# Performance work log

Hardware: AMD Instinct MI355X
Metric: run time of the kernel (lower is better)

Reference implementation:

```python
import jax, jax.numpy as jnp
import numpy as np

N_QUBITS = 10
Q_DEPTH = 6
MAX_LAYERS = 15
DIM = 2 ** N_QUBITS


def _apply_1q(s, U, w):
    # s: (B, 2^n) real statevector (circuit uses only H/RY/CNOT, all real).
    # Wire 0 is the most-significant bit (PennyLane convention).
    a, b = 2 ** w, 2 ** (N_QUBITS - 1 - w)
    s = s.reshape(-1, a, 2, b)
    if U.ndim == 2:  # gate shared across batch
        s = jnp.einsum('ij,Bajb->Baib', U, s)
    else:            # per-sample gate, U: (B,2,2)
        s = jnp.einsum('Bij,Bajb->Baib', U, s)
    return s.reshape(-1, DIM)


def _apply_cnot(s, c, t):
    # CNOT, control c < target t
    s = s.reshape(-1, 2 ** c, 2, 2 ** (t - c - 1), 2, 2 ** (N_QUBITS - 1 - t))
    s = jnp.stack([s[:, :, 0], jnp.flip(s[:, :, 1], axis=3)], axis=2)
    return s.reshape(-1, DIM)


def _ry(theta):
    # RY(theta) = [[cos t/2, -sin t/2], [sin t/2, cos t/2]]; theta scalar or (B,)
    c, si = jnp.cos(theta / 2.0), jnp.sin(theta / 2.0)
    return jnp.stack([jnp.stack([c, -si], -1), jnp.stack([si, c], -1)], -2)


def _quantum_net(q_in, q_params):
    # q_in: (B, n_qubits) rotation angles; q_params: (max_layers*n_qubits,)
    B = q_in.shape[0]
    qw = q_params.reshape(MAX_LAYERS, N_QUBITS)
    s = jnp.zeros((B, DIM), q_in.dtype).at[:, 0].set(1.0)  # |0...0>
    H = jnp.array([[1.0, 1.0], [1.0, -1.0]], q_in.dtype) / jnp.sqrt(jnp.asarray(2.0, q_in.dtype))
    for w in range(N_QUBITS):
        s = _apply_1q(s, H, w)
    for w in range(N_QUBITS):
        s = _apply_1q(s, _ry(q_in[:, w]), w)
    for k in range(Q_DEPTH):
        for i in range(0, N_QUBITS - 1, 2):
            s = _apply_cnot(s, i, i + 1)
        for i in range(1, N_QUBITS - 1, 2):
            s = _apply_cnot(s, i, i + 1)
        for w in range(N_QUBITS):
            s = _apply_1q(s, _ry(qw[k + 1, w]), w)
    probs = s * s
    # <Z_w> = P(bit_w = 0) - P(bit_w = 1)
    z = []
    for w in range(N_QUBITS):
        p = probs.reshape(-1, 2 ** w, 2, 2 ** (N_QUBITS - 1 - w)).sum(axis=(1, 3))
        z.append(p[:, 0] - p[:, 1])
    return jnp.stack(z, axis=1)  # (B, n_qubits)


def setup_inputs() -> dict:
    key = jax.random.key(0)
    ks = jax.random.split(key, 6)
    B, F, NQ, NC = 8192, 512, N_QUBITS, 2
    q_delta = 0.01
    return {
        'input_features': jax.random.normal(ks[0], (B, F), jnp.float32),
        'W_pre': jax.random.normal(ks[1], (NQ, F), jnp.float32) / np.sqrt(F),
        'b_pre': jnp.zeros((NQ,), jnp.float32),
        'q_params': q_delta * jax.random.normal(ks[2], (MAX_LAYERS * NQ,), jnp.float32),
        'W_post': jax.random.normal(ks[3], (NC, NQ), jnp.float32) / np.sqrt(NQ),
        'b_post': jnp.zeros((NC,), jnp.float32),
    }


def reference(input_features, W_pre, b_pre, q_params, W_post, b_post):
    pre_out = input_features @ W_pre.T + b_pre          # (B, n_qubits)
    q_in = jnp.tanh(pre_out) * (np.pi / 2.0)            # scale to [-pi/2, pi/2]
    q_out = _quantum_net(q_in, q_params)                # (B, n_qubits) PauliZ expvals
    return q_out @ W_post.T + b_post                    # (B, n_classes)
```

## Files before the change

kernel.cpp:

```cpp
#include <hip/hip_runtime.h>
#include <math.h>


#define NQ   10
#define NREG 16
#define DIM  1024

typedef _Float16 f16;
typedef _Float16 f16x8 __attribute__((ext_vector_type(8)));
typedef float    f32x4 __attribute__((ext_vector_type(4)));

template<int BB>
__device__ __forceinline__ void ry_lane(float (&s)[NREG], int lane, float c, float si) {
    float sgn = ((lane >> BB) & 1) ? si : -si;
    #pragma unroll
    for (int r = 0; r < NREG; ++r) {
        float o = __shfl_xor(s[r], 1 << BB);
        s[r] = fmaf(sgn, o, c * s[r]);
    }
}
template<int P>
__device__ __forceinline__ void ry_reg(float (&s)[NREG], float c, float si) {
    const int m = 1 << P;
    #pragma unroll
    for (int r = 0; r < NREG; ++r) {
        if ((r & m) == 0) {
            float a = s[r], b = s[r + m];
            s[r]     = fmaf(c, a, -si * b);
            s[r + m] = fmaf(si, a,  c * b);
        }
    }
}
__device__ __forceinline__ void cnot_5_6(float (&s)[NREG], int lane) {
    bool sel = (lane & 1) != 0;
    #pragma unroll
    for (int r = 0; r < 8; ++r) {
        float a = s[r], b = s[r + 8];
        s[r]     = sel ? b : a;
        s[r + 8] = sel ? a : b;
    }
}
template<int PC, int PT>
__device__ __forceinline__ void cnot_reg(float (&s)[NREG]) {
    #pragma unroll
    for (int r = 0; r < NREG; ++r) {
        if (((r >> PC) & 1) && !((r >> PT) & 1)) {
            float t = s[r];
            s[r] = s[r ^ (1 << PT)];
            s[r ^ (1 << PT)] = t;
        }
    }
}
__device__ __forceinline__ void perm_even(float (&s)[NREG], int lane) {
    int src = lane ^ (((((lane >> 5) & 1) << 4)) | ((((lane >> 3) & 1) << 2)) | (((lane >> 1) & 1)));
    #pragma unroll
    for (int r = 0; r < NREG; ++r) s[r] = __shfl(s[r], src);
}
__device__ __forceinline__ void perm_odd(float (&s)[NREG], int lane) {
    int src = lane ^ (((((lane >> 4) & 1) << 3)) | ((((lane >> 2) & 1) << 1)));
    #pragma unroll
    for (int r = 0; r < NREG; ++r) s[r] = __shfl(s[r], src);
}

#define APPLY_RY_ALL(CARR, SARR, BASE)                                        \
    { float c_, s_;                                                           \
      c_=__shfl(CARR,(BASE)+0); s_=__shfl(SARR,(BASE)+0); ry_lane<5>(s,lane,c_,s_); \
      c_=__shfl(CARR,(BASE)+1); s_=__shfl(SARR,(BASE)+1); ry_lane<4>(s,lane,c_,s_); \
      c_=__shfl(CARR,(BASE)+2); s_=__shfl(SARR,(BASE)+2); ry_lane<3>(s,lane,c_,s_); \
      c_=__shfl(CARR,(BASE)+3); s_=__shfl(SARR,(BASE)+3); ry_lane<2>(s,lane,c_,s_); \
      c_=__shfl(CARR,(BASE)+4); s_=__shfl(SARR,(BASE)+4); ry_lane<1>(s,lane,c_,s_); \
      c_=__shfl(CARR,(BASE)+5); s_=__shfl(SARR,(BASE)+5); ry_lane<0>(s,lane,c_,s_); \
      c_=__shfl(CARR,(BASE)+6); s_=__shfl(SARR,(BASE)+6); ry_reg<3>(s,c_,s_);       \
      c_=__shfl(CARR,(BASE)+7); s_=__shfl(SARR,(BASE)+7); ry_reg<2>(s,c_,s_);       \
      c_=__shfl(CARR,(BASE)+8); s_=__shfl(SARR,(BASE)+8); ry_reg<1>(s,c_,s_);       \
      c_=__shfl(CARR,(BASE)+9); s_=__shfl(SARR,(BASE)+9); ry_reg<0>(s,c_,s_); }

__device__ __forceinline__ void async16(const void* g, void* l) {
    __builtin_amdgcn_global_load_lds(
        (const __attribute__((address_space(1))) void*)g,
        (__attribute__((address_space(3))) void*)l, 16, 0, 0);
}

__global__ __launch_bounds__(256) void ka_prepare(
    const float* __restrict__ X, const float* __restrict__ Wpre,
    const float* __restrict__ bpre, const float* __restrict__ qp,
    f16* __restrict__ psi0, f16* __restrict__ Arm, float* __restrict__ z, int B)
{
    const int tid = threadIdx.x, lane = tid & 63, wv = tid >> 6;

    {
        int idx = blockIdx.x * 256 + tid;
        if (idx < 8192 * NQ) z[idx] = 0.0f;
    }

    {
        int sample = blockIdx.x * 4 + wv;
        if (sample < B) {
            const float* xrow = X + (size_t)sample * 512;
            float4 x0 = ((const float4*)xrow)[lane];
            float4 x1 = ((const float4*)xrow)[64 + lane];
            float acc[NQ];
            #pragma unroll
            for (int q = 0; q < NQ; ++q) {
                const float* wr = Wpre + q * 512;
                float4 w0 = ((const float4*)wr)[lane];
                float4 w1 = ((const float4*)wr)[64 + lane];
                float a = x0.x * w0.x;
                a = fmaf(x0.y, w0.y, a); a = fmaf(x0.z, w0.z, a); a = fmaf(x0.w, w0.w, a);
                a = fmaf(x1.x, w1.x, a); a = fmaf(x1.y, w1.y, a);
                a = fmaf(x1.z, w1.z, a); a = fmaf(x1.w, w1.w, a);
                acc[q] = a;
            }
            #pragma unroll
            for (int q = 0; q < NQ; ++q) {
                float v = acc[q];
                #pragma unroll
                for (int d = 32; d >= 1; d >>= 1) v += __shfl_xor(v, d);
                acc[q] = v;
            }
            float pre = acc[0];
            #pragma unroll
            for (int q = 1; q < NQ; ++q) pre = (lane == q) ? acc[q] : pre;
            float c45 = 0.0f, s45 = 0.0f;
            if (lane < NQ) {
                float th = tanhf(pre + bpre[lane]) * 1.5707963267948966f;
                sincosf(0.5f * th + 0.7853981633974483f, &s45, &c45);
            }
            float lv = 1.0f;
            #pragma unroll
            for (int w = 0; w < 6; ++w) {
                float f0 = __shfl(c45, w), f1 = __shfl(s45, w);
                lv *= ((lane >> (5 - w)) & 1) ? f1 : f0;
            }
            float c6 = __shfl(c45, 6), s6 = __shfl(s45, 6);
            float c7 = __shfl(c45, 7), s7 = __shfl(s45, 7);
            float c8 = __shfl(c45, 8), s8 = __shfl(s45, 8);
            float c9 = __shfl(c45, 9), s9 = __shfl(s45, 9);
            float g01[4] = {c6 * c7, c6 * s7, s6 * c7, s6 * s7};
            float g23[4] = {c8 * c9, c8 * s9, s8 * c9, s8 * s9};
            union { f16 h[16]; float4 v[2]; } u;
            #pragma unroll
            for (int r = 0; r < NREG; ++r)
                u.h[r] = (f16)(lv * g01[r >> 2] * g23[r & 3]);
            float4* dst = (float4*)((char*)psi0 + (size_t)sample * 2048 + lane * 32);
            dst[0] = u.v[0];
            dst[1] = u.v[1];
        }
    }

    if (wv < 2) {
        int row = blockIdx.x * 2 + wv;
        if (row < DIM) {
            float cw = 1.0f, swn = 0.0f;
            if (lane < 60) {
                float s_, c_;
                sincosf(0.5f * qp[10 + lane], &s_, &c_);
                cw = c_; swn = -s_;
            }
            float s[NREG];
            int srcLane = row >> 4, srcReg = row & 15;
            #pragma unroll
            for (int r = 0; r < NREG; ++r)
                s[r] = (lane == srcLane && r == srcReg) ? 1.0f : 0.0f;
            for (int kk = 6; kk >= 1; --kk) {
                APPLY_RY_ALL(cw, swn, (kk - 1) * 10);
                perm_odd(s, lane);
                cnot_5_6(s, lane);
                cnot_reg<2, 1>(s);
                perm_even(s, lane);
                cnot_reg<3, 2>(s);
                cnot_reg<1, 0>(s);
            }
            union { f16 h[16]; float4 v[2]; } u;
            #pragma unroll
            for (int r = 0; r < NREG; ++r) u.h[r] = (f16)s[r];
            float4* dst = (float4*)((char*)Arm + (size_t)row * 2048 + lane * 32);
            dst[0] = u.v[0];
            dst[1] = u.v[1];
        }
    }
}

__global__ __launch_bounds__(256) void kb_gemm_measure(
    const f16* __restrict__ psi0, const f16* __restrict__ Arm,
    float* __restrict__ z)
{
    __shared__ __align__(16) char smem[32768];
    const int tid = threadIdx.x, lane = tid & 63, wv = tid >> 6;
    const int mB = blockIdx.x & 63, nB = blockIdx.x >> 6;
    const size_t tM = (size_t)mB * 128, tN = (size_t)nB * 128;
    f16* As = (f16*)smem;
    f16* Bs = (f16*)(smem + 16384);
    const int wm = (wv >> 1) * 64, wn = (wv & 1) * 64;

    f32x4 acc[4][4] = {};

    const f16* ga[4]; const f16* gb[4]; int ldso[4];
    #pragma unroll
    for (int p = 0; p < 4; ++p) {
        int slot = p * 256 + tid;
        int row = slot >> 3, gp = slot & 7, g = gp ^ (row & 7);
        ga[p] = psi0 + (tM + row) * 1024 + g * 8;
        gb[p] = Arm  + (tN + row) * 1024 + g * 8;
        ldso[p] = slot * 16;
    }

    for (int kt = 0; kt < 1024; kt += 64) {
        __syncthreads();
        #pragma unroll
        for (int p = 0; p < 4; ++p) async16(ga[p] + kt, (char*)As + ldso[p]);
        #pragma unroll
        for (int p = 0; p < 4; ++p) async16(gb[p] + kt, (char*)Bs + ldso[p]);
        __syncthreads();
        #pragma unroll
        for (int ks = 0; ks < 2; ++ks) {
            f16x8 af[4], bf[4];
            const int gpb = ks * 4 + (lane >> 4);
            const int gpx = gpb ^ (lane & 7);
            #pragma unroll
            for (int i = 0; i < 4; ++i) {
                int rowA = wm + i * 16 + (lane & 15);
                af[i] = *(const f16x8*)(As + rowA * 64 + gpx * 8);
            }
            #pragma unroll
            for (int j = 0; j < 4; ++j) {
                int rowB = wn + j * 16 + (lane & 15);
                bf[j] = *(const f16x8*)(Bs + rowB * 64 + gpx * 8);
            }
            #pragma unroll
            for (int i = 0; i < 4; ++i)
                #pragma unroll
                for (int j = 0; j < 4; ++j)
                    acc[i][j] = __builtin_amdgcn_mfma_f32_16x16x32_f16(af[i], bf[j], acc[i][j], 0, 0, 0);
        }
    }

    __syncthreads();
    float* zbuf = (float*)smem;
    float* zb = zbuf + (wn ? 1280 : 0);
    const float sg0 = (nB & 4) ? -1.0f : 1.0f;
    const float sg1 = (nB & 2) ? -1.0f : 1.0f;
    const float sg2 = (nB & 1) ? -1.0f : 1.0f;
    const float sg3 = wn ? -1.0f : 1.0f;

    #pragma unroll
    for (int i = 0; i < 4; ++i) {
        #pragma unroll
        for (int t = 0; t < 4; ++t) {
            float p0 = acc[i][0][t] * acc[i][0][t];
            float p1 = acc[i][1][t] * acc[i][1][t];
            float p2 = acc[i][2][t] * acc[i][2][t];
            float p3 = acc[i][3][t] * acc[i][3][t];
            float t0  = (p0 + p1) + (p2 + p3);
            float tw5 = (p0 - p1) + (p2 - p3);
            float tw4 = (p0 + p1) - (p2 + p3);
            float s1 = __shfl_xor(t0, 1);
            float Av = t0 + s1;
            float Bv = (lane & 1) ? s1 - t0 : t0 - s1;
            float sA = __shfl_xor(Av, 2), sB = __shfl_xor(Bv, 2);
            float AP = Av + sA;
            float AM = (lane & 2) ? sA - Av : Av - sA;
            float BP = Bv + sB;
            float sAP = __shfl_xor(AP, 4), sAM = __shfl_xor(AM, 4), sBP = __shfl_xor(BP, 4);
            float APP = AP + sAP;
            float APM = (lane & 4) ? sAP - AP : AP - sAP;
            float AMP = AM + sAM;
            float BPP = BP + sBP;
            float a1 = __shfl_xor(APP, 8), a2 = __shfl_xor(APM, 8);
            float a3 = __shfl_xor(AMP, 8), a4 = __shfl_xor(BPP, 8);
            float T0 = APP + a1;
            float S6 = (lane & 8) ? a1 - APP : APP - a1;
            float S7 = APM + a2;
            float S8 = AMP + a3;
            float S9 = BPP + a4;
            float T5 = tw5, T4 = tw4;
            T5 += __shfl_xor(T5, 1); T5 += __shfl_xor(T5, 2);
            T5 += __shfl_xor(T5, 4); T5 += __shfl_xor(T5, 8);
            T4 += __shfl_xor(T4, 1); T4 += __shfl_xor(T4, 2);
            T4 += __shfl_xor(T4, 4); T4 += __shfl_xor(T4, 8);
            if ((lane & 15) == 0) {
                int row = wm + i * 16 + (lane >> 4) * 4 + t;
                float* d = zb + row * 10;
                d[0] = sg0 * T0; d[1] = sg1 * T0; d[2] = sg2 * T0; d[3] = sg3 * T0;
                d[4] = T4; d[5] = T5;
                d[6] = S6; d[7] = S7; d[8] = S8; d[9] = S9;
            }
        }
    }
    __syncthreads();
    for (int idx = tid; idx < 1280; idx += 256) {
        float v = zbuf[idx] + zbuf[1280 + idx];
        int row = idx / 10, w = idx - row * 10;
        atomicAdd(&z[((size_t)tM + row) * 10 + w], v);
    }
}

__global__ __launch_bounds__(256) void kc_post(
    const float* __restrict__ z, const float* __restrict__ Wpost,
    const float* __restrict__ bpost, float* __restrict__ out, int B)
{
    int gid = blockIdx.x * 256 + threadIdx.x;
    if (gid >= B) return;
    const float* zp = z + (size_t)gid * NQ;
    float o0 = bpost[0], o1 = bpost[1];
    #pragma unroll
    for (int w = 0; w < NQ; ++w) {
        float zw = zp[w];
        o0 = fmaf(zw, Wpost[w], o0);
        o1 = fmaf(zw, Wpost[NQ + w], o1);
    }
    out[(size_t)gid * 2 + 0] = o0;
    out[(size_t)gid * 2 + 1] = o1;
}

template<int BC, int BT>
__device__ __forceinline__ void cnot_lane(float (&s)[NREG], int lane) {
    int src = ((lane >> BC) & 1) ? (lane ^ (1 << BT)) : lane;
    #pragma unroll
    for (int r = 0; r < NREG; ++r) s[r] = __shfl(s[r], src);
}

__global__ __launch_bounds__(256) void hybrid_head_fallback(
    const float* __restrict__ X, const float* __restrict__ Wpre,
    const float* __restrict__ bpre, const float* __restrict__ qp,
    const float* __restrict__ Wpost, const float* __restrict__ bpost,
    float* __restrict__ out, int B)
{
    const int lane = threadIdx.x & 63;
    const int wave = threadIdx.x >> 6;
    const int sample = blockIdx.x * 4 + wave;
    if (sample >= B) return;

    const float* xrow = X + (size_t)sample * 512;
    float4 x0 = ((const float4*)xrow)[lane];
    float4 x1 = ((const float4*)xrow)[64 + lane];
    float acc[NQ];
    #pragma unroll
    for (int q = 0; q < NQ; ++q) {
        const float* wr = Wpre + q * 512;
        float4 w0 = ((const float4*)wr)[lane];
        float4 w1 = ((const float4*)wr)[64 + lane];
        float a = x0.x * w0.x;
        a = fmaf(x0.y, w0.y, a); a = fmaf(x0.z, w0.z, a); a = fmaf(x0.w, w0.w, a);
        a = fmaf(x1.x, w1.x, a); a = fmaf(x1.y, w1.y, a);
        a = fmaf(x1.z, w1.z, a); a = fmaf(x1.w, w1.w, a);
        acc[q] = a;
    }
    #pragma unroll
    for (int q = 0; q < NQ; ++q) {
        float v = acc[q];
        #pragma unroll
        for (int d = 32; d >= 1; d >>= 1) v += __shfl_xor(v, d);
        acc[q] = v;
    }
    float pre = acc[0];
    #pragma unroll
    for (int q = 1; q < NQ; ++q) pre = (lane == q) ? acc[q] : pre;
    float cth = 1.0f, sth = 0.0f;
    if (lane < NQ) {
        float th = tanhf(pre + bpre[lane]) * 1.5707963267948966f;
        sincosf(0.5f * th, &sth, &cth);
    }
    float cw = 1.0f, sw = 0.0f;
    if (lane < 60) sincosf(0.5f * qp[10 + lane], &sw, &cw);

    float s[NREG];
    #pragma unroll
    for (int r = 0; r < NREG; ++r) s[r] = 0.03125f;
    APPLY_RY_ALL(cth, sth, 0);
    for (int k = 0; k < 6; ++k) {
        perm_even(s, lane);
        cnot_reg<3, 2>(s);
        cnot_reg<1, 0>(s);
        perm_odd(s, lane);
        cnot_5_6(s, lane);
        cnot_reg<2, 1>(s);
        APPLY_RY_ALL(cw, sw, k * 10);
    }
    float p[NREG], tot = 0.0f;
    #pragma unroll
    for (int r = 0; r < NREG; ++r) { p[r] = s[r] * s[r]; tot += p[r]; }
    float z[NQ];
    #pragma unroll
    for (int w = 0; w < 6; ++w) z[w] = ((lane >> (5 - w)) & 1) ? -tot : tot;
    z[6] = z[7] = z[8] = z[9] = 0.0f;
    #pragma unroll
    for (int r = 0; r < NREG; ++r) {
        z[6] += ((r >> 3) & 1) ? -p[r] : p[r];
        z[7] += ((r >> 2) & 1) ? -p[r] : p[r];
        z[8] += ((r >> 1) & 1) ? -p[r] : p[r];
        z[9] += ((r >> 0) & 1) ? -p[r] : p[r];
    }
    #pragma unroll
    for (int w = 0; w < NQ; ++w) {
        float v = z[w];
        #pragma unroll
        for (int d = 32; d >= 1; d >>= 1) v += __shfl_xor(v, d);
        z[w] = v;
    }
    if (lane < 2) {
        const float* wp = Wpost + lane * NQ;
        float o = bpost[lane];
        #pragma unroll
        for (int w = 0; w < NQ; ++w) o = fmaf(z[w], wp[w], o);
        out[(size_t)sample * 2 + lane] = o;
    }
}

extern "C" void kernel_launch(void* const* d_in, const int* in_sizes, int n_in,
                              void* d_out, int out_size, void* d_ws, size_t ws_size,
                              hipStream_t stream) {
    const float* X     = (const float*)d_in[0];
    const float* Wpre  = (const float*)d_in[1];
    const float* bpre  = (const float*)d_in[2];
    const float* qp    = (const float*)d_in[3];
    const float* Wpost = (const float*)d_in[4];
    const float* bpost = (const float*)d_in[5];
    float* out = (float*)d_out;
    int B = in_sizes[0] / 512;

    size_t psi0_b = (size_t)B * DIM * sizeof(f16);
    size_t arm_b  = (size_t)DIM * DIM * sizeof(f16);
    size_t z_b    = (size_t)B * NQ * sizeof(float);
    size_t need = psi0_b + arm_b + z_b;

    if (B != 8192 || ws_size < need) {
        hipLaunchKernelGGL(hybrid_head_fallback, dim3((B + 3) / 4), dim3(256), 0, stream,
                           X, Wpre, bpre, qp, Wpost, bpost, out, B);
        return;
    }

    char* ws = (char*)d_ws;
    f16*   psi0 = (f16*)ws;
    f16*   Arm  = (f16*)(ws + psi0_b);
    float* z    = (float*)(ws + psi0_b + arm_b);

    hipLaunchKernelGGL(ka_prepare, dim3(2048), dim3(256), 0, stream,
                       X, Wpre, bpre, qp, psi0, Arm, z, B);
    hipLaunchKernelGGL(kb_gemm_measure, dim3(512), dim3(256), 0, stream,
                       psi0, Arm, z);
    hipLaunchKernelGGL(kc_post, dim3(32), dim3(256), 0, stream,
                       z, Wpost, bpost, out, B);
}
```

Measured before the change: 120.9 us.

## Double-buffer GEMM LDS tiles with async loads overlapping MFMA compute

The GEMM main loop now uses two LDS buffers for A and B. The next k-tile's global-to-LDS async loads are issued before the current tile is computed, with manual vmcnt waits and barriers in place of full syncthreads. The aim is to hide global load latency behind MFMA work. LDS use doubles to 64KB, which may reduce occupancy, and the hand-placed waitcnt makes the code more fragile.

```diff
diff --git a/kernel.cpp b/kernel.cpp
--- a/kernel.cpp
+++ b/kernel.cpp
@@ -81,6 +81,10 @@
         (__attribute__((address_space(3))) void*)l, 16, 0, 0);
 }
 
+#define BARRIER() do { __builtin_amdgcn_s_barrier(); __builtin_amdgcn_sched_barrier(0); } while (0)
+#define VMCNT8()  asm volatile("s_waitcnt vmcnt(8)" ::: "memory")
+#define VMCNT0()  asm volatile("s_waitcnt vmcnt(0)" ::: "memory")
+
 __global__ __launch_bounds__(256) void ka_prepare(
     const float* __restrict__ X, const float* __restrict__ Wpre,
     const float* __restrict__ bpre, const float* __restrict__ qp,
@@ -185,12 +189,14 @@
     const f16* __restrict__ psi0, const f16* __restrict__ Arm,
     float* __restrict__ z)
 {
-    __shared__ __align__(16) char smem[32768];
+    __shared__ __align__(16) char smem[65536];
     const int tid = threadIdx.x, lane = tid & 63, wv = tid >> 6;
     const int mB = blockIdx.x & 63, nB = blockIdx.x >> 6;
     const size_t tM = (size_t)mB * 128, tN = (size_t)nB * 128;
-    f16* As = (f16*)smem;
-    f16* Bs = (f16*)(smem + 16384);
+    f16* As0 = (f16*)smem;
+    f16* Bs0 = (f16*)(smem + 16384);
+    f16* As1 = (f16*)(smem + 32768);
+    f16* Bs1 = (f16*)(smem + 49152);
     const int wm = (wv >> 1) * 64, wn = (wv & 1) * 64;
 
     f32x4 acc[4][4] = {};
@@ -205,13 +211,13 @@
         ldso[p] = slot * 16;
     }
 
-    for (int kt = 0; kt < 1024; kt += 64) {
-        __syncthreads();
-        #pragma unroll
-        for (int p = 0; p < 4; ++p) async16(ga[p] + kt, (char*)As + ldso[p]);
-        #pragma unroll
-        for (int p = 0; p < 4; ++p) async16(gb[p] + kt, (char*)Bs + ldso[p]);
-        __syncthreads();
+    auto stage = [&](f16* Ab, f16* Bb, int kt) {
+        #pragma unroll
+        for (int p = 0; p < 4; ++p) async16(ga[p] + kt, (char*)Ab + ldso[p]);
+        #pragma unroll
+        for (int p = 0; p < 4; ++p) async16(gb[p] + kt, (char*)Bb + ldso[p]);
+    };
+    auto compute = [&](const f16* Ab, const f16* Bb) {
         #pragma unroll
         for (int ks = 0; ks < 2; ++ks) {
             f16x8 af[4], bf[4];
@@ -220,12 +226,12 @@
             #pragma unroll
             for (int i = 0; i < 4; ++i) {
                 int rowA = wm + i * 16 + (lane & 15);
-                af[i] = *(const f16x8*)(As + rowA * 64 + gpx * 8);
+                af[i] = *(const f16x8*)(Ab + rowA * 64 + gpx * 8);
             }
             #pragma unroll
             for (int j = 0; j < 4; ++j) {
                 int rowB = wn + j * 16 + (lane & 15);
-                bf[j] = *(const f16x8*)(Bs + rowB * 64 + gpx * 8);
+                bf[j] = *(const f16x8*)(Bb + rowB * 64 + gpx * 8);
             }
             #pragma unroll
             for (int i = 0; i < 4; ++i)
@@ -233,7 +239,29 @@
                 for (int j = 0; j < 4; ++j)
                     acc[i][j] = __builtin_amdgcn_mfma_f32_16x16x32_f16(af[i], bf[j], acc[i][j], 0, 0, 0);
         }
-    }
+    };
+
+    stage(As0, Bs0, 0);
+    #pragma unroll 1
+    for (int kt = 0; kt < 896; kt += 128) {
+        stage(As1, Bs1, kt + 64);
+        VMCNT8();
+        BARRIER();
+        compute(As0, Bs0);
+        BARRIER();
+        stage(As0, Bs0, kt + 128);
+        VMCNT8();
+        BARRIER();
+        compute(As1, Bs1);
+        BARRIER();
+    }
+    stage(As1, Bs1, 960);
+    VMCNT8();
+    BARRIER();
+    compute(As0, Bs0);
+    VMCNT0();
+    BARRIER();
+    compute(As1, Bs1);
 
     __syncthreads();
     float* zbuf = (float*)smem;
```

Result: faster. 118.4 us (-2.1%).
